# Kernel tuning notes

Hardware: AMD Instinct MI355X
Metric: run time of the kernel (lower is better)

Reference implementation:

```python
import jax, jax.numpy as jnp
import numpy as np

D = 2048
N_SLOTS = 8
ALPHA_MIN = 0.02
FAST_DECAY = 0.95
ALPHA_BOOST = 1.0
B = 16384


def setup_inputs() -> dict:
    key = jax.random.key(0)
    ks = jax.random.split(key, 12)
    h = jax.random.normal(ks[0], (B, D), dtype=jnp.float32)
    neighbor_msg = jax.random.normal(ks[1], (B, D), dtype=jnp.float32)
    keys = jax.random.normal(ks[2], (N_SLOTS, D), dtype=jnp.float32) / (D ** 0.5)
    # torch nn.Linear convention: W [out, in], y = x @ W.T + b
    Wr = jax.random.normal(ks[3], (D, D), dtype=jnp.float32) * 0.02
    br = jnp.zeros((D,), dtype=jnp.float32)
    Wc = jax.random.normal(ks[4], (2, 2 * D), dtype=jnp.float32) * 0.02
    bc = jnp.zeros((2,), dtype=jnp.float32)
    Ww = jax.random.normal(ks[5], (D, 2 * D), dtype=jnp.float32) * 0.02
    bw = jnp.zeros((D,), dtype=jnp.float32)
    state = jax.random.normal(ks[6], (N_SLOTS, D), dtype=jnp.float32) * 0.1
    fast = jax.random.normal(ks[7], (N_SLOTS, D), dtype=jnp.float32) * 0.1
    return {"h": h, "neighbor_msg": neighbor_msg, "keys": keys,
            "Wr": Wr, "br": br, "Wc": Wc, "bc": bc, "Ww": Ww, "bw": bw,
            "state": state, "fast": fast}


def reference(h, neighbor_msg, keys, Wr, br, Wc, bc, Ww, bw, state, fast):
    # read_proj
    q = h @ Wr.T + br                                  # [B, D]
    attn = jax.nn.softmax(q @ keys.T, axis=-1)         # [B, n_slots]
    read = attn @ (state + fast)                       # [B, D]
    # ctrl -> add/erase gates (erase computed but unused downstream, as in source)
    ctrl = jnp.concatenate([h, read], axis=-1) @ Wc.T + bc   # [B, 2]
    add = jax.nn.sigmoid(ctrl[:, 0:1])
    erase = jax.nn.sigmoid(ctrl[:, 1:2])
    alpha = jnp.clip(ALPHA_MIN + (1.0 - ALPHA_MIN) * jnp.mean(add), 0.0, 1.0)
    alpha = jnp.clip(alpha * ALPHA_BOOST, 0.0, 1.0)
    # attention-weighted write into slots
    w_in = jnp.concatenate([h + neighbor_msg, read], axis=-1)  # [B, 2D]
    delta = attn.T @ (w_in @ Ww.T + bw)                # [n_slots, D]
    new_state = (1.0 - alpha) * state + alpha * delta
    new_fast = FAST_DECAY * fast + (1.0 - FAST_DECAY) * delta
    return read, attn, alpha, new_state, new_fast
```

## Files before the change

### kernel.cpp

```cpp
#include <hip/hip_runtime.h>
#include <math.h>

#define D 2048
#define NS 8
#define BTOT 16384

#define ATTN_OFF  ((size_t)BTOT * D)
#define ALPHA_OFF (ATTN_OFF + (size_t)BTOT * NS)
#define STATE_OFF (ALPHA_OFF + 1)
#define FAST_OFF  (STATE_OFF + (size_t)NS * D)

#define WS_SM    0
#define WS_KPX   16384
#define WS_PB    34816
#define WS_LB    51200
#define WS_SWC   51208
#define WS_GALL  51216

__global__ void __launch_bounds__(256) kZ(const float* __restrict__ st, const float* __restrict__ fa,
                                          const float* __restrict__ Wc, float* __restrict__ ws) {
  int i = blockIdx.x * 256 + threadIdx.x;
  if (i < 16384) {
    ws[WS_SM + i] = st[i] + fa[i];
  } else if (i < 32768) {
    ws[WS_KPX + (i - 16384)] = 0.f;
  } else if (i < 34816) {
    ws[WS_KPX + 16384 + (i - 32768)] = Wc[i - 32768];
  } else if (i < 51200) {
    ws[WS_PB + (i - 34816)] = 0.f;
  } else if (i < 51264) {
    ws[WS_LB + (i - 51200)] = 0.f;
  }
}

__global__ void __launch_bounds__(256) kA(const float* __restrict__ keys,
                                          const float* __restrict__ Wr,
                                          float* __restrict__ kpx) {
  int e = blockIdx.x * 256 + threadIdx.x;
  int d0 = blockIdx.y * 64;
  float acc[NS] = {0.f,0.f,0.f,0.f,0.f,0.f,0.f,0.f};
  for (int d = d0; d < d0 + 64; ++d) {
    float wv = Wr[(size_t)d * D + e];
#pragma unroll
    for (int s = 0; s < NS; ++s) acc[s] += keys[s * D + d] * wv;
  }
#pragma unroll
  for (int s = 0; s < NS; ++s) atomicAdd(&kpx[s * D + e], acc[s]);
}

__global__ void __launch_bounds__(256) kC(const float* __restrict__ keys,
                                          const float* __restrict__ br,
                                          const float* __restrict__ Wc,
                                          const float* __restrict__ sm,
                                          float* __restrict__ lb, float* __restrict__ swc) {
  int t = threadIdx.x;
  int idx = blockIdx.x * 256 + t;
  float brv = br[idx];
  float wcr = Wc[D + idx];
  float v[16];
#pragma unroll
  for (int s = 0; s < NS; ++s) {
    v[s]     = keys[s * D + idx] * brv;
    v[8 + s] = sm[s * D + idx] * wcr;
  }
#pragma unroll
  for (int off = 32; off > 0; off >>= 1) {
#pragma unroll
    for (int k = 0; k < 16; ++k) v[k] += __shfl_down(v[k], off);
  }
  __shared__ float red[4 * 16];
  int lane = t & 63, wid = t >> 6;
  if (lane == 0) {
#pragma unroll
    for (int k = 0; k < 16; ++k) red[wid * 16 + k] = v[k];
  }
  __syncthreads();
  if (t < 16) {
    float tot = red[t] + red[16 + t] + red[32 + t] + red[48 + t];
    if (t < 8) atomicAdd(&lb[t], tot); else atomicAdd(&swc[t - 8], tot);
  }
}

__global__ void __launch_bounds__(256, 4) k1r(const float* __restrict__ h,
                                              const float* __restrict__ kpx,
                                              const float* __restrict__ lb, const float* __restrict__ swc,
                                              const float* __restrict__ bc,
                                              float* __restrict__ attn, float* __restrict__ gall) {
  int t = threadIdx.x;
  int q = t & 15;
  int row = blockIdx.x * 16 + (t >> 4);
  const float4* h4 = (const float4*)h + (size_t)row * 512;
  const float4* kp4 = (const float4*)kpx;
  float acc[9] = {0.f,0.f,0.f,0.f,0.f,0.f,0.f,0.f,0.f};
#pragma unroll 4
  for (int j = 0; j < 32; ++j) {
    float4 hv = h4[j * 16 + q];
#pragma unroll
    for (int s = 0; s < 9; ++s) {
      float4 kv = kp4[s * 512 + j * 16 + q];
      acc[s] += hv.x * kv.x + hv.y * kv.y + hv.z * kv.z + hv.w * kv.w;
    }
  }
#pragma unroll
  for (int off = 1; off <= 8; off <<= 1) {
#pragma unroll
    for (int s = 0; s < 9; ++s) acc[s] += __shfl_xor(acc[s], off);
  }
  float lg[8]; float m = -1e30f;
#pragma unroll
  for (int s = 0; s < NS; ++s) { lg[s] = acc[s] + lb[s]; m = fmaxf(m, lg[s]); }
  float sum = 0.f;
#pragma unroll
  for (int s = 0; s < NS; ++s) { lg[s] = expf(lg[s] - m); sum += lg[s]; }
  float inv = 1.f / sum;
  float x = acc[8] + bc[0];
#pragma unroll
  for (int s = 0; s < NS; ++s) { lg[s] *= inv; x += lg[s] * swc[s]; }
  float add = 1.f / (1.f + expf(-x));
  if (q == 0) ((float4*)(attn + (size_t)row * NS))[0] = make_float4(lg[0], lg[1], lg[2], lg[3]);
  if (q == 1) ((float4*)(attn + (size_t)row * NS))[1] = make_float4(lg[4], lg[5], lg[6], lg[7]);
  float v[45];
  {
    int c = 0;
#pragma unroll
    for (int i = 0; i < NS; ++i)
#pragma unroll
      for (int j = i; j < NS; ++j) v[c++] = lg[i] * lg[j];
  }
#pragma unroll
  for (int s = 0; s < NS; ++s) v[36 + s] = lg[s];
  v[44] = add;
#pragma unroll
  for (int off = 16; off <= 32; off <<= 1) {
#pragma unroll
    for (int k = 0; k < 45; ++k) v[k] += __shfl_xor(v[k], off);
  }
  __shared__ float red[4][45];
  int lane = t & 63, w = t >> 6;
  if (lane == 0) {
#pragma unroll
    for (int k = 0; k < 45; ++k) red[w][k] = v[k];
  }
  __syncthreads();
  if (t < 45) {
    float tot = red[0][t] + red[1][t] + red[2][t] + red[3][t];
    atomicAdd(&gall[t], tot);
  }
}

static __device__ __forceinline__ float4 f4fma(float s, float4 a, float4 c) {
  c.x += s * a.x; c.y += s * a.y; c.z += s * a.z; c.w += s * a.w; return c;
}

__global__ void __launch_bounds__(256, 4) k2n(const float* __restrict__ h, const float* __restrict__ nm,
                                              const float* __restrict__ sm, const float* __restrict__ attn,
                                              float* __restrict__ readout, float* __restrict__ pb) {
  __shared__ float4 lp[8][NS][32];
  int t = threadIdx.x;
  int c4 = t & 31, r4 = t >> 5;
  int chunk = blockIdx.x, rc = blockIdx.y;
  int fbase = chunk * 32 + c4;
  const float4* sm4 = (const float4*)sm;
  float4 S[NS];
#pragma unroll
  for (int s = 0; s < NS; ++s) S[s] = sm4[s * 512 + fbase];
  float4 P[NS];
#pragma unroll
  for (int s = 0; s < NS; ++s) P[s] = make_float4(0.f, 0.f, 0.f, 0.f);
  int rowbase = rc * 256;
#pragma unroll 2
  for (int it = 0; it < 32; ++it) {
    int row = rowbase + it * 8 + r4;
    float4 hv = ((const float4*)h)[(size_t)row * 512 + fbase];
    float4 nv = ((const float4*)nm)[(size_t)row * 512 + fbase];
    const float* ar = attn + (size_t)row * NS;
    float a[NS];
#pragma unroll
    for (int s = 0; s < NS; ++s) a[s] = ar[s];
    float4 wv = make_float4(hv.x + nv.x, hv.y + nv.y, hv.z + nv.z, hv.w + nv.w);
    float4 rd = make_float4(0.f, 0.f, 0.f, 0.f);
#pragma unroll
    for (int s = 0; s < NS; ++s) {
      rd = f4fma(a[s], S[s], rd);
      P[s] = f4fma(a[s], wv, P[s]);
    }
    ((float4*)readout)[(size_t)row * 512 + fbase] = rd;
  }
#pragma unroll
  for (int s = 0; s < NS; ++s) lp[r4][s][c4] = P[s];
  __syncthreads();
  {
    int s = t >> 5, c = t & 31;
    float4 v = make_float4(0.f, 0.f, 0.f, 0.f);
#pragma unroll
    for (int g = 0; g < 8; ++g) {
      float4 u = lp[g][s][c];
      v.x += u.x; v.y += u.y; v.z += u.z; v.w += u.w;
    }
    float* dst = pb + s * D + chunk * 128 + c * 4;
    atomicAdd(dst + 0, v.x); atomicAdd(dst + 1, v.y);
    atomicAdd(dst + 2, v.z); atomicAdd(dst + 3, v.w);
  }
}

__global__ void __launch_bounds__(256) k4(const float* __restrict__ Ww, const float* __restrict__ bw,
                                          const float* __restrict__ st, const float* __restrict__ fa,
                                          const float* __restrict__ p, const float* __restrict__ sm,
                                          const float* __restrict__ gall,
                                          float* __restrict__ outst, float* __restrict__ outfa,
                                          float* __restrict__ alphaout) {
  int dd = blockIdx.x, t = threadIdx.x;
  const float4* wr = (const float4*)(Ww + (size_t)dd * (2 * D));
  float4 w0 = wr[t], w1 = wr[256 + t], w2 = wr[512 + t], w3 = wr[768 + t];
  const float4* p4 = (const float4*)p;
  const float4* s4 = (const float4*)sm;
  float acc[16];
#pragma unroll
  for (int s = 0; s < NS; ++s) {
    float4 pa = p4[s * 512 + t], pb2 = p4[s * 512 + 256 + t];
    float4 sa = s4[s * 512 + t], sb = s4[s * 512 + 256 + t];
    acc[s] = w0.x * pa.x + w0.y * pa.y + w0.z * pa.z + w0.w * pa.w
           + w1.x * pb2.x + w1.y * pb2.y + w1.z * pb2.z + w1.w * pb2.w;
    acc[8 + s] = w2.x * sa.x + w2.y * sa.y + w2.z * sa.z + w2.w * sa.w
               + w3.x * sb.x + w3.y * sb.y + w3.z * sb.z + w3.w * sb.w;
  }
#pragma unroll
  for (int off = 32; off > 0; off >>= 1) {
#pragma unroll
    for (int k = 0; k < 16; ++k) acc[k] += __shfl_down(acc[k], off);
  }
  __shared__ float red[4][16];
  __shared__ float red2[16];
  int lane = t & 63, wid = t >> 6;
  if (lane == 0) {
#pragma unroll
    for (int k = 0; k < 16; ++k) red[wid][k] = acc[k];
  }
  __syncthreads();
  if (t < 16) red2[t] = red[0][t] + red[1][t] + red[2][t] + red[3][t];
  __syncthreads();
  if (t < NS) {
    float delta = red2[t];
#pragma unroll
    for (int sp = 0; sp < NS; ++sp) {
      int i = t < sp ? t : sp;
      int j = t < sp ? sp : t;
      int idx = i * 8 - (i * (i - 1)) / 2 + (j - i);
      delta += gall[idx] * red2[8 + sp];
    }
    delta += gall[36 + t] * bw[dd];
    float al = 0.02f + 0.98f * (gall[44] * (1.f / (float)BTOT));
    al = fminf(fmaxf(al, 0.f), 1.f);
    size_t idx2 = (size_t)t * D + dd;
    outst[idx2] = (1.f - al) * st[idx2] + al * delta;
    outfa[idx2] = 0.95f * fa[idx2] + 0.05f * delta;
  }
  if (dd == 0 && t == 0) {
    float al = 0.02f + 0.98f * (gall[44] * (1.f / (float)BTOT));
    alphaout[0] = fminf(fmaxf(al, 0.f), 1.f);
  }
}

extern "C" void kernel_launch(void* const* d_in, const int* in_sizes, int n_in,
                              void* d_out, int out_size, void* d_ws, size_t ws_size,
                              hipStream_t stream) {
  const float* h    = (const float*)d_in[0];
  const float* nm   = (const float*)d_in[1];
  const float* keys = (const float*)d_in[2];
  const float* Wr   = (const float*)d_in[3];
  const float* br   = (const float*)d_in[4];
  const float* Wc   = (const float*)d_in[5];
  const float* bc   = (const float*)d_in[6];
  const float* Ww   = (const float*)d_in[7];
  const float* bw   = (const float*)d_in[8];
  const float* st   = (const float*)d_in[9];
  const float* fa   = (const float*)d_in[10];
  float* out = (float*)d_out;
  float* ws  = (float*)d_ws;

  float* sm   = ws + WS_SM;
  float* kpx  = ws + WS_KPX;
  float* pb   = ws + WS_PB;
  float* lb   = ws + WS_LB;
  float* swc  = ws + WS_SWC;
  float* gall = ws + WS_GALL;
  float* attn = out + ATTN_OFF;

  kZ<<<201, 256, 0, stream>>>(st, fa, Wc, ws);
  kA<<<dim3(8, 32), 256, 0, stream>>>(keys, Wr, kpx);
  kC<<<8, 256, 0, stream>>>(keys, br, Wc, sm, lb, swc);
  k1r<<<1024, 256, 0, stream>>>(h, kpx, lb, swc, bc, attn, gall);
  k2n<<<dim3(16, 64), 256, 0, stream>>>(h, nm, sm, attn, out, pb);
  k4<<<2048, 256, 0, stream>>>(Ww, bw, st, fa, pb, sm, gall, out + STATE_OFF, out + FAST_OFF,
                               out + ALPHA_OFF);
}
```

Baseline: 444.5 us.

## Fold bias reductions into init kernel and prefetch rows in k1r and k2n

Removes the separate kC launch by computing the key-bias and Wc read-column reductions in an extra block of the init kernel, writing them directly without atomics. k1r now loads the whole h row slice into registers up front and drops its occupancy hint from 4 to 3. k2n software-pipelines its row loop by prefetching the next row's h, neighbor and attention values, and reads attention as float4. These changes aim to cut launch overhead and hide global load latency, at the cost of higher register pressure and lower occupancy. The init kernel also now zeroes the gall accumulator explicitly.

Result: slower. 657.9 us (+48.0%).

```diff
diff --git a/kernel.cpp b/kernel.cpp
--- a/kernel.cpp
+++ b/kernel.cpp
@@ -18,8 +18,43 @@
 #define WS_GALL  51216
 
 __global__ void __launch_bounds__(256) kZ(const float* __restrict__ st, const float* __restrict__ fa,
-                                          const float* __restrict__ Wc, float* __restrict__ ws) {
-  int i = blockIdx.x * 256 + threadIdx.x;
+                                          const float* __restrict__ Wc,
+                                          const float* __restrict__ keys, const float* __restrict__ br,
+                                          float* __restrict__ ws) {
+  int t = threadIdx.x;
+  if (blockIdx.x == 201) {
+    float v[16];
+#pragma unroll
+    for (int k = 0; k < 16; ++k) v[k] = 0.f;
+    for (int k = 0; k < 8; ++k) {
+      int idx = k * 256 + t;
+      float brv = br[idx];
+      float wcr = Wc[D + idx];
+#pragma unroll
+      for (int s = 0; s < NS; ++s) {
+        v[s]     += keys[s * D + idx] * brv;
+        v[8 + s] += (st[s * D + idx] + fa[s * D + idx]) * wcr;
+      }
+    }
+#pragma unroll
+    for (int off = 32; off > 0; off >>= 1) {
+#pragma unroll
+      for (int k = 0; k < 16; ++k) v[k] += __shfl_down(v[k], off);
+    }
+    __shared__ float red[4 * 16];
+    int lane = t & 63, wid = t >> 6;
+    if (lane == 0) {
+#pragma unroll
+      for (int k = 0; k < 16; ++k) red[wid * 16 + k] = v[k];
+    }
+    __syncthreads();
+    if (t < 16) {
+      float tot = red[t] + red[16 + t] + red[32 + t] + red[48 + t];
+      if (t < 8) ws[WS_LB + t] = tot; else ws[WS_SWC + (t - 8)] = tot;
+    }
+    return;
+  }
+  int i = blockIdx.x * 256 + t;
   if (i < 16384) {
     ws[WS_SM + i] = st[i] + fa[i];
   } else if (i < 32768) {
@@ -28,8 +63,8 @@
     ws[WS_KPX + 16384 + (i - 32768)] = Wc[i - 32768];
   } else if (i < 51200) {
     ws[WS_PB + (i - 34816)] = 0.f;
-  } else if (i < 51264) {
-    ws[WS_LB + (i - 51200)] = 0.f;
+  } else if (i < 51248) {
+    ws[WS_GALL + (i - 51200)] = 0.f;
   }
 }
 
@@ -48,40 +83,7 @@
   for (int s = 0; s < NS; ++s) atomicAdd(&kpx[s * D + e], acc[s]);
 }
 
-__global__ void __launch_bounds__(256) kC(const float* __restrict__ keys,
-                                          const float* __restrict__ br,
-                                          const float* __restrict__ Wc,
-                                          const float* __restrict__ sm,
-                                          float* __restrict__ lb, float* __restrict__ swc) {
-  int t = threadIdx.x;
-  int idx = blockIdx.x * 256 + t;
-  float brv = br[idx];
-  float wcr = Wc[D + idx];
-  float v[16];
-#pragma unroll
-  for (int s = 0; s < NS; ++s) {
-    v[s]     = keys[s * D + idx] * brv;
-    v[8 + s] = sm[s * D + idx] * wcr;
-  }
-#pragma unroll
-  for (int off = 32; off > 0; off >>= 1) {
-#pragma unroll
-    for (int k = 0; k < 16; ++k) v[k] += __shfl_down(v[k], off);
-  }
-  __shared__ float red[4 * 16];
-  int lane = t & 63, wid = t >> 6;
-  if (lane == 0) {
-#pragma unroll
-    for (int k = 0; k < 16; ++k) red[wid * 16 + k] = v[k];
-  }
-  __syncthreads();
-  if (t < 16) {
-    float tot = red[t] + red[16 + t] + red[32 + t] + red[48 + t];
-    if (t < 8) atomicAdd(&lb[t], tot); else atomicAdd(&swc[t - 8], tot);
-  }
-}
-
-__global__ void __launch_bounds__(256, 4) k1r(const float* __restrict__ h,
+__global__ void __launch_bounds__(256, 3) k1r(const float* __restrict__ h,
                                               const float* __restrict__ kpx,
                                               const float* __restrict__ lb, const float* __restrict__ swc,
                                               const float* __restrict__ bc,
@@ -91,14 +93,16 @@
   int row = blockIdx.x * 16 + (t >> 4);
   const float4* h4 = (const float4*)h + (size_t)row * 512;
   const float4* kp4 = (const float4*)kpx;
+  float4 hv[32];
+#pragma unroll
+  for (int j = 0; j < 32; ++j) hv[j] = h4[j * 16 + q];
   float acc[9] = {0.f,0.f,0.f,0.f,0.f,0.f,0.f,0.f,0.f};
-#pragma unroll 4
+#pragma unroll
   for (int j = 0; j < 32; ++j) {
-    float4 hv = h4[j * 16 + q];
 #pragma unroll
     for (int s = 0; s < 9; ++s) {
       float4 kv = kp4[s * 512 + j * 16 + q];
-      acc[s] += hv.x * kv.x + hv.y * kv.y + hv.z * kv.z + hv.w * kv.w;
+      acc[s] += hv[j].x * kv.x + hv[j].y * kv.y + hv[j].z * kv.z + hv[j].w * kv.w;
     }
   }
 #pragma unroll
@@ -161,22 +165,32 @@
   int chunk = blockIdx.x, rc = blockIdx.y;
   int fbase = chunk * 32 + c4;
   const float4* sm4 = (const float4*)sm;
+  const float4* h4 = (const float4*)h;
+  const float4* nm4 = (const float4*)nm;
+  const float4* at4 = (const float4*)attn;
+  float4* rd4 = (float4*)readout;
   float4 S[NS];
 #pragma unroll
   for (int s = 0; s < NS; ++s) S[s] = sm4[s * 512 + fbase];
   float4 P[NS];
 #pragma unroll
   for (int s = 0; s < NS; ++s) P[s] = make_float4(0.f, 0.f, 0.f, 0.f);
-  int rowbase = rc * 256;
-#pragma unroll 2
+  int row = rc * 256 + r4;
+  float4 hv = h4[(size_t)row * 512 + fbase];
+  float4 nv = nm4[(size_t)row * 512 + fbase];
+  float4 a0 = at4[(size_t)row * 2];
+  float4 a1 = at4[(size_t)row * 2 + 1];
+#pragma unroll 4
   for (int it = 0; it < 32; ++it) {
-    int row = rowbase + it * 8 + r4;
-    float4 hv = ((const float4*)h)[(size_t)row * 512 + fbase];
-    float4 nv = ((const float4*)nm)[(size_t)row * 512 + fbase];
-    const float* ar = attn + (size_t)row * NS;
-    float a[NS];
-#pragma unroll
-    for (int s = 0; s < NS; ++s) a[s] = ar[s];
+    float4 hn, nn, b0, b1;
+    if (it < 31) {
+      int nrow = row + 8;
+      hn = h4[(size_t)nrow * 512 + fbase];
+      nn = nm4[(size_t)nrow * 512 + fbase];
+      b0 = at4[(size_t)nrow * 2];
+      b1 = at4[(size_t)nrow * 2 + 1];
+    }
+    float a[NS] = {a0.x, a0.y, a0.z, a0.w, a1.x, a1.y, a1.z, a1.w};
     float4 wv = make_float4(hv.x + nv.x, hv.y + nv.y, hv.z + nv.z, hv.w + nv.w);
     float4 rd = make_float4(0.f, 0.f, 0.f, 0.f);
 #pragma unroll
@@ -184,7 +198,8 @@
       rd = f4fma(a[s], S[s], rd);
       P[s] = f4fma(a[s], wv, P[s]);
     }
-    ((float4*)readout)[(size_t)row * 512 + fbase] = rd;
+    rd4[(size_t)row * 512 + fbase] = rd;
+    row += 8; hv = hn; nv = nn; a0 = b0; a1 = b1;
   }
 #pragma unroll
   for (int s = 0; s < NS; ++s) lp[r4][s][c4] = P[s];
@@ -286,9 +301,8 @@
   float* gall = ws + WS_GALL;
   float* attn = out + ATTN_OFF;
 
-  kZ<<<201, 256, 0, stream>>>(st, fa, Wc, ws);
+  kZ<<<202, 256, 0, stream>>>(st, fa, Wc, keys, br, ws);
   kA<<<dim3(8, 32), 256, 0, stream>>>(keys, Wr, kpx);
-  kC<<<8, 256, 0, stream>>>(keys, br, Wc, sm, lb, swc);
   k1r<<<1024, 256, 0, stream>>>(h, kpx, lb, swc, bc, attn, gall);
   k2n<<<dim3(16, 64), 256, 0, stream>>>(h, nm, sm, attn, out, pb);
   k4<<<2048, 256, 0, stream>>>(Ww, bw, st, fa, pb, sm, gall, out + STATE_OFF, out + FAST_OFF,
```
